# Optimization experiments

Hardware: AMD Instinct MI355X
Metric: run time of the kernel (lower is better)

The kernel has to match this reference:

```python
import jax, jax.numpy as jnp
import numpy as np

N = 50000      # nodes
E = 800000     # edges
F_IN = 512     # input feature dim
H1 = 8         # heads layer 1
F_HID = 8      # per-head hidden dim (concat -> 64)
H2 = 1         # heads layer 2
NLAB = 64      # output classes
LRELU_SLOPE = 0.2


def setup_inputs() -> dict:
    key = jax.random.key(0)
    ks = jax.random.split(key, 9)
    inputs = jax.random.normal(ks[0], (N, F_IN), jnp.float32)
    src = jax.random.randint(ks[1], (E,), 0, N, dtype=jnp.int32)
    dst = jax.random.randint(ks[2], (E,), 0, N, dtype=jnp.int32)
    s1 = 1.0 / np.sqrt(F_IN)
    s2 = 1.0 / np.sqrt(H1 * F_HID)
    W1 = jax.random.normal(ks[3], (H1, F_IN, F_HID), jnp.float32) * s1
    a1_src = jax.random.normal(ks[4], (H1, F_HID), jnp.float32) * 0.1
    a1_dst = jax.random.normal(ks[5], (H1, F_HID), jnp.float32) * 0.1
    W2 = jax.random.normal(ks[6], (H2, H1 * F_HID, NLAB), jnp.float32) * s2
    a2_src = jax.random.normal(ks[7], (H2, NLAB), jnp.float32) * 0.1
    a2_dst = jax.random.normal(ks[8], (H2, NLAB), jnp.float32) * 0.1
    return {"inputs": inputs, "W1": W1, "a1_src": a1_src, "a1_dst": a1_dst,
            "W2": W2, "a2_src": a2_src, "a2_dst": a2_dst, "src": src, "dst": dst}


def gat_layer(x, W, a_s, a_d, src, dst):
    # x: [N, F]; W: [H, F, O]; a_s/a_d: [H, O]
    Wh = jnp.einsum('nf,hfo->nho', x, W)                    # [N, H, O]
    es = jnp.einsum('nho,ho->nh', Wh, a_s)                  # [N, H]
    ed = jnp.einsum('nho,ho->nh', Wh, a_d)                  # [N, H]
    e = jax.nn.leaky_relu(es[src] + ed[dst], LRELU_SLOPE)   # [E, H]
    # neighborhood softmax over incoming edges of each dst node
    m = jax.lax.stop_gradient(jax.ops.segment_max(e, dst, num_segments=N))
    ex = jnp.exp(e - m[dst])                                # [E, H]
    den = jax.ops.segment_sum(ex, dst, num_segments=N)      # [N, H]
    alpha = ex / (den[dst] + 1e-10)                         # [E, H]
    msgs = alpha[:, :, None] * Wh[src]                      # [E, H, O]
    return jax.ops.segment_sum(msgs, dst, num_segments=N)   # [N, H, O]


def reference(inputs, W1, a1_src, a1_dst, W2, a2_src, a2_dst, src, dst):
    # eval mode: dropout rate 0, identity
    h = gat_layer(inputs, W1, a1_src, a1_dst, src, dst)     # [N, H1, F_HID]
    h = jax.nn.elu(h.reshape(N, H1 * F_HID))                # concat heads (reduction=False)
    o = gat_layer(h, W2, a2_src, a2_dst, src, dst)          # [N, H2, NLAB]
    o = o.mean(axis=1)                                      # average heads (reduction=True)
    return jax.nn.softmax(o, axis=-1)                       # [N, NLAB] (squeezed)
```

## Files before the change

### kernel.cpp

```cpp
#include <hip/hip_runtime.h>
#include <math.h>

#define N_NODES 50000
#define N_EDGES 800000
#define F_IN    512
#define H1      8
#define F_HID   8
#define C1      64
#define NLAB    64
#define SLOPE   0.2f
#define MAXDEG  64
#define DEGS    16

#define NBLK_WT   128
#define NBLK_Z    782
#define NBLK_G1   782
#define REC1     160
#define REC2     144

typedef __attribute__((ext_vector_type(8))) short short8;
typedef __attribute__((ext_vector_type(4))) float f32x4;

__device__ __forceinline__ float bf_lo(unsigned u) { return __uint_as_float(u << 16); }
__device__ __forceinline__ float bf_hi(unsigned u) { return __uint_as_float(u & 0xFFFF0000u); }
__device__ __forceinline__ unsigned short f2bf(float x) {
    unsigned bits = __float_as_uint(x);
    return (unsigned short)((bits + 0x7FFF + ((bits >> 16) & 1)) >> 16);
}

__global__ void k_prep(const float* __restrict__ W1, unsigned short* __restrict__ Bh,
                       unsigned short* __restrict__ Bl, int* __restrict__ deg) {
    int b = blockIdx.x;
    if (b < NBLK_WT) {
        int i = b * 256 + threadIdx.x;
        int c = i >> 9, f = i & 511;
        float v = W1[(c >> 3) * (F_IN * F_HID) + f * F_HID + (c & 7)];
        unsigned bits = __float_as_uint(v);
        float r = v - __uint_as_float(bits & 0xFFFF0000u);
        Bh[i] = (unsigned short)(bits >> 16);
        Bl[i] = (unsigned short)(__float_as_uint(r) >> 16);
    } else {
        int i = (b - NBLK_WT) * 256 + threadIdx.x;
        if (i < N_NODES * DEGS / 4)
            *(int4*)(deg + i * 4) = make_int4(0, 0, 0, 0);
    }
}

__launch_bounds__(256)
__global__ void k_gemm1f(const float* __restrict__ X, const unsigned short* __restrict__ Bh,
                         const unsigned short* __restrict__ Bl, const float* __restrict__ a_s,
                         const float* __restrict__ a_d, char* __restrict__ rec,
                         float* __restrict__ ed,
                         const int* __restrict__ src, const int* __restrict__ dst,
                         int* __restrict__ deg, int* __restrict__ colPad) {
    __shared__ unsigned short sBh[64][136];
    __shared__ unsigned short sBl[64][136];

    const int b = blockIdx.x;
    const int g = b / 5, r = b % 5;
    if (r) {
        int e = (g * 4 + (r - 1)) * 256 + threadIdx.x;
        if (e >= N_EDGES) return;
        int d = dst[e];
        int s = src[e];
        int slot = atomicAdd(&deg[d << 4], 1);
        colPad[(d << 6) | min(slot, MAXDEG - 1)] = s;
        return;
    }

    const int t = threadIdx.x;
    const int lane = t & 63, w = t >> 6;
    const int r0 = g * 64 + w * 16;
    const int m = lane & 15, quad = lane >> 4;
    int row = r0 + m; if (row >= N_NODES) row = N_NODES - 1;
    const float* xrow = X + (size_t)row * F_IN + quad * 8;

    const int sc = t >> 2;
    const int sp = t & 3;

    f32x4 acc[4] = {};
    float4 pxa[4], pxb[4];
    #pragma unroll
    for (int i = 0; i < 4; i++) {
        pxa[i] = *(const float4*)(xrow + i * 32);
        pxb[i] = *(const float4*)(xrow + i * 32 + 4);
    }

    for (int chunk = 0; chunk < 4; chunk++) {
        const int k0 = chunk * 128;
        if (chunk) __syncthreads();
        #pragma unroll
        for (int i = 0; i < 4; i++) {
            *(short8*)(&sBh[sc][sp * 32 + i * 8]) =
                *(const short8*)(Bh + sc * F_IN + k0 + sp * 32 + i * 8);
            *(short8*)(&sBl[sc][sp * 32 + i * 8]) =
                *(const short8*)(Bl + sc * F_IN + k0 + sp * 32 + i * 8);
        }
        __syncthreads();
        #pragma unroll
        for (int i = 0; i < 4; i++) {
            float xs[8] = {pxa[i].x, pxa[i].y, pxa[i].z, pxa[i].w,
                           pxb[i].x, pxb[i].y, pxb[i].z, pxb[i].w};
            if (chunk < 3) {
                const int ktn = k0 + 128 + i * 32;
                pxa[i] = *(const float4*)(xrow + ktn);
                pxb[i] = *(const float4*)(xrow + ktn + 4);
            }
            short8 ah, al;
            #pragma unroll
            for (int j = 0; j < 8; j++) {
                unsigned bits = __float_as_uint(xs[j]);
                float rr = xs[j] - __uint_as_float(bits & 0xFFFF0000u);
                ah[j] = (short)(bits >> 16);
                al[j] = (short)(__float_as_uint(rr) >> 16);
            }
            #pragma unroll
            for (int s = 0; s < 4; s++) {
                short8 bh = *(const short8*)(&sBh[s * 16 + m][i * 32 + quad * 8]);
                short8 bl = *(const short8*)(&sBl[s * 16 + m][i * 32 + quad * 8]);
                acc[s] = __builtin_amdgcn_mfma_f32_16x16x32_bf16(al, bh, acc[s], 0, 0, 0);
                acc[s] = __builtin_amdgcn_mfma_f32_16x16x32_bf16(ah, bl, acc[s], 0, 0, 0);
                acc[s] = __builtin_amdgcn_mfma_f32_16x16x32_bf16(ah, bh, acc[s], 0, 0, 0);
            }
        }
    }
    __syncthreads();
    unsigned short* sWh = &sBh[0][0] + w * 1024;
    #pragma unroll
    for (int s = 0; s < 4; s++)
        #pragma unroll
        for (int reg = 0; reg < 4; reg++)
            sWh[(quad * 4 + reg) * 64 + s * 16 + m] = f2bf(acc[s][reg]);
    __syncthreads();
    const int rr = lane & 15, p = lane >> 4;
    const int n = r0 + rr;
    if (n >= N_NODES) return;
    float es2v[2], edv[2];
    #pragma unroll
    for (int hh = 0; hh < 2; hh++) {
        int h = 2 * p + hh;
        float s = 0.f, dsum = 0.f;
        #pragma unroll
        for (int j = 0; j < 8; j++) {
            float v = __uint_as_float((unsigned)sWh[rr * 64 + h * 8 + j] << 16);
            s += v * a_s[h * 8 + j];
            dsum += v * a_d[h * 8 + j];
        }
        es2v[hh] = s; edv[hh] = dsum;
    }
    char* rp = rec + (size_t)n * REC1;
    *(float2*)(rp + p * 8) = make_float2(es2v[0], es2v[1]);
    *(short8*)(rp + 32 + p * 32)      = *(const short8*)(sWh + rr * 64 + p * 16);
    *(short8*)(rp + 32 + p * 32 + 16) = *(const short8*)(sWh + rr * 64 + p * 16 + 8);
    *(float2*)(ed + n * 8 + 2 * p) = make_float2(edv[0], edv[1]);
}

__launch_bounds__(256)
__global__ void k_agg1g2(const char* __restrict__ rec, const float* __restrict__ ed,
                         const int* __restrict__ deg, const int* __restrict__ colPad,
                         const float* __restrict__ W2, const float* __restrict__ a2s,
                         const float* __restrict__ a2d,
                         char* __restrict__ rec2, float* __restrict__ ed2) {
    __shared__ float Ws[64 * 64];
    __shared__ float hs[32][64];
    const int t = threadIdx.x;
    #pragma unroll
    for (int i = 0; i < 4; i++) {
        int flat = i * 256 + t;
        *(float4*)(Ws + flat * 4) = *(const float4*)(W2 + flat * 4);
    }
    const int n0 = blockIdx.x * 32;
    const int n = n0 + (t >> 3), q = t & 7;

    float o[8] = {};
    if (n < N_NODES) {
        int d = deg[n << 4];
        int start = n << 6;
        float edq = ed[n * 8 + q];
        float den = 0.f;
        float acc[8] = {};
        for (int e = 0; e < d; e += 2) {
            int sv0 = colPad[start + e];
            int sv1 = colPad[start + min(e + 1, d - 1)];
            const char* r0 = rec + (size_t)sv0 * REC1;
            const char* r1 = rec + (size_t)sv1 * REC1;
            float x0 = *(const float*)(r0 + q * 4) + edq;
            float x1 = *(const float*)(r1 + q * 4) + edq;
            uint4 u0 = *(const uint4*)(r0 + 32 + q * 16);
            uint4 u1 = *(const uint4*)(r1 + 32 + q * 16);
            x0 = x0 > 0.f ? x0 : SLOPE * x0;
            x1 = x1 > 0.f ? x1 : SLOPE * x1;
            float w0 = __expf(x0);
            float w1 = (e + 1 < d) ? __expf(x1) : 0.f;
            den += w0 + w1;
            float f0[8] = {bf_lo(u0.x), bf_hi(u0.x), bf_lo(u0.y), bf_hi(u0.y),
                           bf_lo(u0.z), bf_hi(u0.z), bf_lo(u0.w), bf_hi(u0.w)};
            float f1[8] = {bf_lo(u1.x), bf_hi(u1.x), bf_lo(u1.y), bf_hi(u1.y),
                           bf_lo(u1.z), bf_hi(u1.z), bf_lo(u1.w), bf_hi(u1.w)};
            #pragma unroll
            for (int j = 0; j < 8; j++) acc[j] += w0 * f0[j] + w1 * f1[j];
        }
        float inv = 1.f / (den + 1e-10f);
        #pragma unroll
        for (int j = 0; j < 8; j++) {
            float v = acc[j] * inv;
            o[j] = v > 0.f ? v : expm1f(v);
        }
    }
    float4* hp = (float4*)(&hs[t >> 3][q * 8]);
    hp[0] = make_float4(o[0], o[1], o[2], o[3]);
    hp[1] = make_float4(o[4], o[5], o[6], o[7]);
    __syncthreads();

    const int wv = t >> 6, lane = t & 63;
    float as = a2s[lane], ad = a2d[lane];
    #pragma unroll
    for (int j = 0; j < 8; j++) {
        int nl = wv * 8 + j;
        int nn = n0 + nl;
        if (nn >= N_NODES) break;
        float acc = 0.f;
        #pragma unroll
        for (int k = 0; k < 64; k++) acc += hs[nl][k] * Ws[k * 64 + lane];
        char* r = rec2 + (size_t)nn * REC2;
        *(unsigned short*)(r + 16 + lane * 2) = f2bf(acc);
        float s = acc * as;
        float dd = acc * ad;
        #pragma unroll
        for (int off = 1; off < 64; off <<= 1) {
            s += __shfl_xor(s, off);
            dd += __shfl_xor(dd, off);
        }
        if (lane == 0) { *(float*)r = s; ed2[nn] = dd; }
    }
}

__launch_bounds__(256)
__global__ void k_agg2(const char* __restrict__ rec2, const float* __restrict__ ed2,
                       const int* __restrict__ deg, const int* __restrict__ colPad,
                       float* __restrict__ out) {
    int tid = blockIdx.x * 256 + threadIdx.x;
    int n = tid >> 3, q = tid & 7;
    if (n >= N_NODES) return;
    int d = deg[n << 4];
    int start = n << 6;
    float edn = ed2[n];

    float den = 0.f;
    float acc[8] = {};
    for (int e = 0; e < d; e += 2) {
        int sv0 = colPad[start + e];
        int sv1 = colPad[start + min(e + 1, d - 1)];
        const char* r0 = rec2 + (size_t)sv0 * REC2;
        const char* r1 = rec2 + (size_t)sv1 * REC2;
        float x0 = *(const float*)r0 + edn;
        float x1 = *(const float*)r1 + edn;
        uint4 u0 = *(const uint4*)(r0 + 16 + q * 16);
        uint4 u1 = *(const uint4*)(r1 + 16 + q * 16);
        x0 = x0 > 0.f ? x0 : SLOPE * x0;
        x1 = x1 > 0.f ? x1 : SLOPE * x1;
        float w0 = __expf(x0);
        float w1 = (e + 1 < d) ? __expf(x1) : 0.f;
        den += w0 + w1;
        float f0[8] = {bf_lo(u0.x), bf_hi(u0.x), bf_lo(u0.y), bf_hi(u0.y),
                       bf_lo(u0.z), bf_hi(u0.z), bf_lo(u0.w), bf_hi(u0.w)};
        float f1[8] = {bf_lo(u1.x), bf_hi(u1.x), bf_lo(u1.y), bf_hi(u1.y),
                       bf_lo(u1.z), bf_hi(u1.z), bf_lo(u1.w), bf_hi(u1.w)};
        #pragma unroll
        for (int j = 0; j < 8; j++) acc[j] += w0 * f0[j] + w1 * f1[j];
    }
    float inv = 1.f / (den + 1e-10f);
    float o[8];
    #pragma unroll
    for (int j = 0; j < 8; j++) o[j] = acc[j] * inv;
    float mx = o[0];
    #pragma unroll
    for (int j = 1; j < 8; j++) mx = fmaxf(mx, o[j]);
    mx = fmaxf(mx, __shfl_xor(mx, 1));
    mx = fmaxf(mx, __shfl_xor(mx, 2));
    mx = fmaxf(mx, __shfl_xor(mx, 4));
    float e8[8], sm = 0.f;
    #pragma unroll
    for (int j = 0; j < 8; j++) { e8[j] = __expf(o[j] - mx); sm += e8[j]; }
    sm += __shfl_xor(sm, 1);
    sm += __shfl_xor(sm, 2);
    sm += __shfl_xor(sm, 4);
    float inv2 = 1.f / sm;
    float4* op = (float4*)(out + (size_t)n * 64 + q * 8);
    op[0] = make_float4(e8[0] * inv2, e8[1] * inv2, e8[2] * inv2, e8[3] * inv2);
    op[1] = make_float4(e8[4] * inv2, e8[5] * inv2, e8[6] * inv2, e8[7] * inv2);
}

extern "C" void kernel_launch(void* const* d_in, const int* in_sizes, int n_in,
                              void* d_out, int out_size, void* d_ws, size_t ws_size,
                              hipStream_t stream) {
    const float* X   = (const float*)d_in[0];
    const float* W1  = (const float*)d_in[1];
    const float* a1s = (const float*)d_in[2];
    const float* a1d = (const float*)d_in[3];
    const float* W2  = (const float*)d_in[4];
    const float* a2s = (const float*)d_in[5];
    const float* a2d = (const float*)d_in[6];
    const int*   src = (const int*)d_in[7];
    const int*   dst = (const int*)d_in[8];
    float* out = (float*)d_out;

    char* w = (char*)d_ws;
    size_t off = 0;
    auto alloc = [&](size_t bytes) {
        void* p = w + off;
        off += (bytes + 255) & ~(size_t)255;
        return p;
    };
    unsigned short* Bh  = (unsigned short*)alloc((size_t)C1 * F_IN * 2);
    unsigned short* Bl  = (unsigned short*)alloc((size_t)C1 * F_IN * 2);
    char*  rec1  = (char*)alloc((size_t)N_NODES * REC1);
    char*  rec2  = (char*)alloc((size_t)N_NODES * REC2);
    float* ed1   = (float*)alloc((size_t)N_NODES * 8 * 4);
    float* ed2   = (float*)alloc((size_t)N_NODES * 4);
    int*   deg   = (int*)alloc((size_t)N_NODES * DEGS * 4);
    int*   colPad= (int*)alloc((size_t)N_NODES * MAXDEG * 4);

    k_prep<<<NBLK_WT + NBLK_Z, 256, 0, stream>>>(W1, Bh, Bl, deg);
    k_gemm1f<<<NBLK_G1 * 5, 256, 0, stream>>>(X, Bh, Bl, a1s, a1d, rec1, ed1,
                                              src, dst, deg, colPad);
    k_agg1g2<<<(N_NODES + 31) / 32, 256, 0, stream>>>(rec1, ed1, deg, colPad,
                                                      W2, a2s, a2d, rec2, ed2);
    k_agg2<<<(N_NODES * 8 + 255) / 256, 256, 0, stream>>>(rec2, ed2, deg, colPad, out);
}
```

Before: 281.0 us.

## Bin edges by destination range before building padded adjacency; split node records

Graph construction becomes a two-pass binning. A prep kernel histograms edges into 98 bins of 512 destination nodes and scatters (dst,src) pairs into per-bin buffers. Then one block per bin builds colPad and degree counts using shared-memory atomics instead of global atomics on scattered deg entries. Node records are split into separate es/wh arrays. The aggregation loops load the neighbor list with vector loads and broadcast indices by shuffle, unrolled over 64 fixed slots with predication. This adds a memset and an intermediate edge buffer, and the fixed 64-slot unroll issues predicated work even for low-degree nodes.

```diff
diff --git a/kernel.cpp b/kernel.cpp
--- a/kernel.cpp
+++ b/kernel.cpp
@@ -10,13 +10,12 @@
 #define NLAB    64
 #define SLOPE   0.2f
 #define MAXDEG  64
-#define DEGS    16
-
-#define NBLK_WT   128
-#define NBLK_Z    782
-#define NBLK_G1   782
-#define REC1     160
-#define REC2     144
+
+#define NBIN    98
+#define BINCAP  9216
+#define NBLK_WT  128
+#define NBLK_E   196
+#define NBLK_G1  782
 
 typedef __attribute__((ext_vector_type(8))) short short8;
 typedef __attribute__((ext_vector_type(4))) float f32x4;
@@ -29,7 +28,9 @@
 }
 
 __global__ void k_prep(const float* __restrict__ W1, unsigned short* __restrict__ Bh,
-                       unsigned short* __restrict__ Bl, int* __restrict__ deg) {
+                       unsigned short* __restrict__ Bl,
+                       const int* __restrict__ src, const int* __restrict__ dst,
+                       int2* __restrict__ ebuf, int* __restrict__ gctr) {
     int b = blockIdx.x;
     if (b < NBLK_WT) {
         int i = b * 256 + threadIdx.x;
@@ -39,38 +40,82 @@
         float r = v - __uint_as_float(bits & 0xFFFF0000u);
         Bh[i] = (unsigned short)(bits >> 16);
         Bl[i] = (unsigned short)(__float_as_uint(r) >> 16);
-    } else {
-        int i = (b - NBLK_WT) * 256 + threadIdx.x;
-        if (i < N_NODES * DEGS / 4)
-            *(int4*)(deg + i * 4) = make_int4(0, 0, 0, 0);
+        return;
+    }
+    __shared__ int hist[NBIN];
+    __shared__ int cur[NBIN];
+    const int t = threadIdx.x;
+    const int eb = b - NBLK_WT;
+    if (t < NBIN) hist[t] = 0;
+    __syncthreads();
+    int4 dv[4], sv[4];
+    const int e0 = eb * 4096 + t * 4;
+    #pragma unroll
+    for (int i = 0; i < 4; i++) {
+        int e = e0 + i * 1024;
+        if (e < N_EDGES) {
+            dv[i] = *(const int4*)(dst + e);
+            sv[i] = *(const int4*)(src + e);
+            atomicAdd(&hist[dv[i].x >> 9], 1);
+            atomicAdd(&hist[dv[i].y >> 9], 1);
+            atomicAdd(&hist[dv[i].z >> 9], 1);
+            atomicAdd(&hist[dv[i].w >> 9], 1);
+        }
+    }
+    __syncthreads();
+    if (t < NBIN) cur[t] = atomicAdd(&gctr[t], hist[t]);
+    __syncthreads();
+    #pragma unroll
+    for (int i = 0; i < 4; i++) {
+        int e = e0 + i * 1024;
+        if (e < N_EDGES) {
+            int d, s, sl;
+            d = dv[i].x; s = sv[i].x; sl = atomicAdd(&cur[d >> 9], 1);
+            ebuf[(size_t)(d >> 9) * BINCAP + min(sl, BINCAP - 1)] = make_int2(d, s);
+            d = dv[i].y; s = sv[i].y; sl = atomicAdd(&cur[d >> 9], 1);
+            ebuf[(size_t)(d >> 9) * BINCAP + min(sl, BINCAP - 1)] = make_int2(d, s);
+            d = dv[i].z; s = sv[i].z; sl = atomicAdd(&cur[d >> 9], 1);
+            ebuf[(size_t)(d >> 9) * BINCAP + min(sl, BINCAP - 1)] = make_int2(d, s);
+            d = dv[i].w; s = sv[i].w; sl = atomicAdd(&cur[d >> 9], 1);
+            ebuf[(size_t)(d >> 9) * BINCAP + min(sl, BINCAP - 1)] = make_int2(d, s);
+        }
     }
 }
 
 __launch_bounds__(256)
 __global__ void k_gemm1f(const float* __restrict__ X, const unsigned short* __restrict__ Bh,
                          const unsigned short* __restrict__ Bl, const float* __restrict__ a_s,
-                         const float* __restrict__ a_d, char* __restrict__ rec,
-                         float* __restrict__ ed,
-                         const int* __restrict__ src, const int* __restrict__ dst,
+                         const float* __restrict__ a_d, float* __restrict__ es1,
+                         unsigned short* __restrict__ wh1, float* __restrict__ ed,
+                         const int2* __restrict__ ebuf, const int* __restrict__ gctr,
                          int* __restrict__ deg, int* __restrict__ colPad) {
     __shared__ unsigned short sBh[64][136];
     __shared__ unsigned short sBl[64][136];
 
     const int b = blockIdx.x;
-    const int g = b / 5, r = b % 5;
-    if (r) {
-        int e = (g * 4 + (r - 1)) * 256 + threadIdx.x;
-        if (e >= N_EDGES) return;
-        int d = dst[e];
-        int s = src[e];
-        int slot = atomicAdd(&deg[d << 4], 1);
-        colPad[(d << 6) | min(slot, MAXDEG - 1)] = s;
+    const int t = threadIdx.x;
+    if (b < NBIN) {
+        int* cnt = (int*)&sBh[0][0];
+        const int lo = b << 9;
+        const int cnum = min(gctr[b], BINCAP);
+        for (int i = t; i < 512; i += 256) cnt[i] = 0;
+        __syncthreads();
+        const int2* eb2 = ebuf + (size_t)b * BINCAP;
+        for (int i = t; i < cnum; i += 256) {
+            int2 e = eb2[i];
+            int sl = atomicAdd(&cnt[e.x - lo], 1);
+            colPad[(e.x << 6) | min(sl, MAXDEG - 1)] = e.y;
+        }
+        __syncthreads();
+        for (int i = t; i < 512; i += 256) {
+            int n = lo + i;
+            if (n < N_NODES) deg[n] = min(cnt[i], MAXDEG);
+        }
         return;
     }
 
-    const int t = threadIdx.x;
     const int lane = t & 63, w = t >> 6;
-    const int r0 = g * 64 + w * 16;
+    const int r0 = (b - NBIN) * 64 + w * 16;
     const int m = lane & 15, quad = lane >> 4;
     int row = r0 + m; if (row >= N_NODES) row = N_NODES - 1;
     const float* xrow = X + (size_t)row * F_IN + quad * 8;
@@ -148,19 +193,20 @@
         }
         es2v[hh] = s; edv[hh] = dsum;
     }
-    char* rp = rec + (size_t)n * REC1;
-    *(float2*)(rp + p * 8) = make_float2(es2v[0], es2v[1]);
-    *(short8*)(rp + 32 + p * 32)      = *(const short8*)(sWh + rr * 64 + p * 16);
-    *(short8*)(rp + 32 + p * 32 + 16) = *(const short8*)(sWh + rr * 64 + p * 16 + 8);
+    *(float2*)(es1 + n * 8 + 2 * p) = make_float2(es2v[0], es2v[1]);
+    *(short8*)(wh1 + (size_t)n * 64 + p * 16)     = *(const short8*)(sWh + rr * 64 + p * 16);
+    *(short8*)(wh1 + (size_t)n * 64 + p * 16 + 8) = *(const short8*)(sWh + rr * 64 + p * 16 + 8);
     *(float2*)(ed + n * 8 + 2 * p) = make_float2(edv[0], edv[1]);
 }
 
 __launch_bounds__(256)
-__global__ void k_agg1g2(const char* __restrict__ rec, const float* __restrict__ ed,
+__global__ void k_agg1g2(const float* __restrict__ es1, const unsigned short* __restrict__ wh1,
+                         const float* __restrict__ ed,
                          const int* __restrict__ deg, const int* __restrict__ colPad,
                          const float* __restrict__ W2, const float* __restrict__ a2s,
                          const float* __restrict__ a2d,
-                         char* __restrict__ rec2, float* __restrict__ ed2) {
+                         float* __restrict__ es2, unsigned short* __restrict__ wh2,
+                         float* __restrict__ ed2) {
     __shared__ float Ws[64 * 64];
     __shared__ float hs[32][64];
     const int t = threadIdx.x;
@@ -171,34 +217,49 @@
     }
     const int n0 = blockIdx.x * 32;
     const int n = n0 + (t >> 3), q = t & 7;
+    const int gb = (t & 63) & 56;
 
     float o[8] = {};
     if (n < N_NODES) {
-        int d = deg[n << 4];
-        int start = n << 6;
+        const int d = deg[n];
+        const int base = n << 6;
+        int4 c0 = *(const int4*)(colPad + base + q * 4);
+        int4 c1 = *(const int4*)(colPad + base + 32 + q * 4);
         float edq = ed[n * 8 + q];
         float den = 0.f;
         float acc[8] = {};
-        for (int e = 0; e < d; e += 2) {
-            int sv0 = colPad[start + e];
-            int sv1 = colPad[start + min(e + 1, d - 1)];
-            const char* r0 = rec + (size_t)sv0 * REC1;
-            const char* r1 = rec + (size_t)sv1 * REC1;
-            float x0 = *(const float*)(r0 + q * 4) + edq;
-            float x1 = *(const float*)(r1 + q * 4) + edq;
-            uint4 u0 = *(const uint4*)(r0 + 32 + q * 16);
-            uint4 u1 = *(const uint4*)(r1 + 32 + q * 16);
-            x0 = x0 > 0.f ? x0 : SLOPE * x0;
-            x1 = x1 > 0.f ? x1 : SLOPE * x1;
-            float w0 = __expf(x0);
-            float w1 = (e + 1 < d) ? __expf(x1) : 0.f;
-            den += w0 + w1;
-            float f0[8] = {bf_lo(u0.x), bf_hi(u0.x), bf_lo(u0.y), bf_hi(u0.y),
-                           bf_lo(u0.z), bf_hi(u0.z), bf_lo(u0.w), bf_hi(u0.w)};
-            float f1[8] = {bf_lo(u1.x), bf_hi(u1.x), bf_lo(u1.y), bf_hi(u1.y),
-                           bf_lo(u1.z), bf_hi(u1.z), bf_lo(u1.w), bf_hi(u1.w)};
+        #pragma unroll
+        for (int comp = 0; comp < 4; comp++) {
+            int m0 = (comp == 0) ? c0.x : (comp == 1) ? c0.y : (comp == 2) ? c0.z : c0.w;
+            int m1 = (comp == 0) ? c1.x : (comp == 1) ? c1.y : (comp == 2) ? c1.z : c1.w;
             #pragma unroll
-            for (int j = 0; j < 8; j++) acc[j] += w0 * f0[j] + w1 * f1[j];
+            for (int srcl = 0; srcl < 8; srcl++) {
+                int sv0 = __shfl(m0, gb + srcl);
+                int sv1 = __shfl(m1, gb + srcl);
+                int i0 = srcl * 4 + comp;
+                if (i0 < d) {
+                    float x = es1[sv0 * 8 + q] + edq;
+                    uint4 u = *(const uint4*)(wh1 + (size_t)sv0 * 64 + q * 8);
+                    x = x > 0.f ? x : SLOPE * x;
+                    float wg = __expf(x);
+                    den += wg;
+                    acc[0] += wg * bf_lo(u.x); acc[1] += wg * bf_hi(u.x);
+                    acc[2] += wg * bf_lo(u.y); acc[3] += wg * bf_hi(u.y);
+                    acc[4] += wg * bf_lo(u.z); acc[5] += wg * bf_hi(u.z);
+                    acc[6] += wg * bf_lo(u.w); acc[7] += wg * bf_hi(u.w);
+                }
+                if (i0 + 32 < d) {
+                    float x = es1[sv1 * 8 + q] + edq;
+                    uint4 u = *(const uint4*)(wh1 + (size_t)sv1 * 64 + q * 8);
+                    x = x > 0.f ? x : SLOPE * x;
+                    float wg = __expf(x);
+                    den += wg;
+                    acc[0] += wg * bf_lo(u.x); acc[1] += wg * bf_hi(u.x);
+                    acc[2] += wg * bf_lo(u.y); acc[3] += wg * bf_hi(u.y);
+                    acc[4] += wg * bf_lo(u.z); acc[5] += wg * bf_hi(u.z);
+                    acc[6] += wg * bf_lo(u.w); acc[7] += wg * bf_hi(u.w);
+                }
+            }
         }
         float inv = 1.f / (den + 1e-10f);
         #pragma unroll
@@ -222,8 +283,7 @@
         float acc = 0.f;
         #pragma unroll
         for (int k = 0; k < 64; k++) acc += hs[nl][k] * Ws[k * 64 + lane];
-        char* r = rec2 + (size_t)nn * REC2;
-        *(unsigned short*)(r + 16 + lane * 2) = f2bf(acc);
+        wh2[(size_t)nn * 64 + lane] = f2bf(acc);
         float s = acc * as;
         float dd = acc * ad;
         #pragma unroll
@@ -231,43 +291,60 @@
             s += __shfl_xor(s, off);
             dd += __shfl_xor(dd, off);
         }
-        if (lane == 0) { *(float*)r = s; ed2[nn] = dd; }
+        if (lane == 0) { es2[nn] = s; ed2[nn] = dd; }
     }
 }
 
 __launch_bounds__(256)
-__global__ void k_agg2(const char* __restrict__ rec2, const float* __restrict__ ed2,
+__global__ void k_agg2(const float* __restrict__ es2, const unsigned short* __restrict__ wh2,
+                       const float* __restrict__ ed2,
                        const int* __restrict__ deg, const int* __restrict__ colPad,
                        float* __restrict__ out) {
     int tid = blockIdx.x * 256 + threadIdx.x;
     int n = tid >> 3, q = tid & 7;
     if (n >= N_NODES) return;
-    int d = deg[n << 4];
-    int start = n << 6;
+    const int t = threadIdx.x;
+    const int gb = (t & 63) & 56;
+    const int d = deg[n];
+    const int base = n << 6;
+    int4 c0 = *(const int4*)(colPad + base + q * 4);
+    int4 c1 = *(const int4*)(colPad + base + 32 + q * 4);
     float edn = ed2[n];
 
     float den = 0.f;
     float acc[8] = {};
-    for (int e = 0; e < d; e += 2) {
-        int sv0 = colPad[start + e];
-        int sv1 = colPad[start + min(e + 1, d - 1)];
-        const char* r0 = rec2 + (size_t)sv0 * REC2;
-        const char* r1 = rec2 + (size_t)sv1 * REC2;
-        float x0 = *(const float*)r0 + edn;
-        float x1 = *(const float*)r1 + edn;
-        uint4 u0 = *(const uint4*)(r0 + 16 + q * 16);
-        uint4 u1 = *(const uint4*)(r1 + 16 + q * 16);
-        x0 = x0 > 0.f ? x0 : SLOPE * x0;
-        x1 = x1 > 0.f ? x1 : SLOPE * x1;
-        float w0 = __expf(x0);
-        float w1 = (e + 1 < d) ? __expf(x1) : 0.f;
-        den += w0 + w1;
-        float f0[8] = {bf_lo(u0.x), bf_hi(u0.x), bf_lo(u0.y), bf_hi(u0.y),
-                       bf_lo(u0.z), bf_hi(u0.z), bf_lo(u0.w), bf_hi(u0.w)};
-        float f1[8] = {bf_lo(u1.x), bf_hi(u1.x), bf_lo(u1.y), bf_hi(u1.y),
-                       bf_lo(u1.z), bf_hi(u1.z), bf_lo(u1.w), bf_hi(u1.w)};
-        #pragma unroll
-        for (int j = 0; j < 8; j++) acc[j] += w0 * f0[j] + w1 * f1[j];
+    #pragma unroll
+    for (int comp = 0; comp < 4; comp++) {
+        int m0 = (comp == 0) ? c0.x : (comp == 1) ? c0.y : (comp == 2) ? c0.z : c0.w;
+        int m1 = (comp == 0) ? c1.x : (comp == 1) ? c1.y : (comp == 2) ? c1.z : c1.w;
+        #pragma unroll
+        for (int srcl = 0; srcl < 8; srcl++) {
+            int sv0 = __shfl(m0, gb + srcl);
+            int sv1 = __shfl(m1, gb + srcl);
+            int i0 = srcl * 4 + comp;
+            if (i0 < d) {
+                float x = es2[sv0] + edn;
+                uint4 u = *(const uint4*)(wh2 + (size_t)sv0 * 64 + q * 8);
+                x = x > 0.f ? x : SLOPE * x;
+                float wg = __expf(x);
+                den += wg;
+                acc[0] += wg * bf_lo(u.x); acc[1] += wg * bf_hi(u.x);
+                acc[2] += wg * bf_lo(u.y); acc[3] += wg * bf_hi(u.y);
+                acc[4] += wg * bf_lo(u.z); acc[5] += wg * bf_hi(u.z);
+                acc[6] += wg * bf_lo(u.w); acc[7] += wg * bf_hi(u.w);
+            }
+            if (i0 + 32 < d) {
+                float x = es2[sv1] + edn;
+                uint4 u = *(const uint4*)(wh2 + (size_t)sv1 * 64 + q * 8);
+                x = x > 0.f ? x : SLOPE * x;
+                float wg = __expf(x);
+                den += wg;
+                acc[0] += wg * bf_lo(u.x); acc[1] += wg * bf_hi(u.x);
+                acc[2] += wg * bf_lo(u.y); acc[3] += wg * bf_hi(u.y);
+                acc[4] += wg * bf_lo(u.z); acc[5] += wg * bf_hi(u.z);
+                acc[6] += wg * bf_lo(u.w); acc[7] += wg * bf_hi(u.w);
+            }
+        }
     }
     float inv = 1.f / (den + 1e-10f);
     float o[8];
@@ -312,19 +389,25 @@
         off += (bytes + 255) & ~(size_t)255;
         return p;
     };
-    unsigned short* Bh  = (unsigned short*)alloc((size_t)C1 * F_IN * 2);
-    unsigned short* Bl  = (unsigned short*)alloc((size_t)C1 * F_IN * 2);
-    char*  rec1  = (char*)alloc((size_t)N_NODES * REC1);
-    char*  rec2  = (char*)alloc((size_t)N_NODES * REC2);
-    float* ed1   = (float*)alloc((size_t)N_NODES * 8 * 4);
-    float* ed2   = (float*)alloc((size_t)N_NODES * 4);
-    int*   deg   = (int*)alloc((size_t)N_NODES * DEGS * 4);
-    int*   colPad= (int*)alloc((size_t)N_NODES * MAXDEG * 4);
-
-    k_prep<<<NBLK_WT + NBLK_Z, 256, 0, stream>>>(W1, Bh, Bl, deg);
-    k_gemm1f<<<NBLK_G1 * 5, 256, 0, stream>>>(X, Bh, Bl, a1s, a1d, rec1, ed1,
-                                              src, dst, deg, colPad);
-    k_agg1g2<<<(N_NODES + 31) / 32, 256, 0, stream>>>(rec1, ed1, deg, colPad,
-                                                      W2, a2s, a2d, rec2, ed2);
-    k_agg2<<<(N_NODES * 8 + 255) / 256, 256, 0, stream>>>(rec2, ed2, deg, colPad, out);
-}
+    unsigned short* Bh   = (unsigned short*)alloc((size_t)C1 * F_IN * 2);
+    unsigned short* Bl   = (unsigned short*)alloc((size_t)C1 * F_IN * 2);
+    float*          es1  = (float*)alloc((size_t)N_NODES * 8 * 4);
+    unsigned short* wh1  = (unsigned short*)alloc((size_t)N_NODES * 64 * 2);
+    float*          es2  = (float*)alloc((size_t)N_NODES * 4);
+    unsigned short* wh2  = (unsigned short*)alloc((size_t)N_NODES * 64 * 2);
+    float*          ed1  = (float*)alloc((size_t)N_NODES * 8 * 4);
+    float*          ed2  = (float*)alloc((size_t)N_NODES * 4);
+    int*            deg  = (int*)alloc((size_t)N_NODES * 4);
+    int*            colPad = (int*)alloc((size_t)N_NODES * MAXDEG * 4);
+    int2*           ebuf = (int2*)alloc((size_t)NBIN * BINCAP * 8);
+    int*            gctr = (int*)alloc((size_t)NBIN * 4);
+
+    hipMemsetAsync(gctr, 0, NBIN * 4, stream);
+
+    k_prep<<<NBLK_WT + NBLK_E, 256, 0, stream>>>(W1, Bh, Bl, src, dst, ebuf, gctr);
+    k_gemm1f<<<NBIN + NBLK_G1, 256, 0, stream>>>(X, Bh, Bl, a1s, a1d, es1, wh1, ed1,
+                                                 ebuf, gctr, deg, colPad);
+    k_agg1g2<<<(N_NODES + 31) / 32, 256, 0, stream>>>(es1, wh1, ed1, deg, colPad,
+                                                      W2, a2s, a2d, es2, wh2, ed2);
+    k_agg2<<<(N_NODES * 8 + 255) / 256, 256, 0, stream>>>(es2, wh2, ed2, deg, colPad, out);
+}
```

New measurement: 274.0 us. -2.5%, faster.
